# Kernel optimization log

Hardware: AMD Instinct MI355X
Metric: run time of the kernel (lower is better)

## Reference

```python
import jax, jax.numpy as jnp
import numpy as np

H = 8  # hidden size (hardcoded in the module)


def _lstm_scan(x, Wih, Whh, b):
    """Unidirectional LSTM over x:[B,T,I] with PyTorch gate order (i,f,g,o).
    Wih:[4H,I], Whh:[4H,H], b:[4H] (= b_ih + b_hh). Returns h seq [B,T,H]."""
    B = x.shape[0]
    # Precompute input projections for all timesteps in one GEMM: [T,B,4H]
    xg = jnp.einsum('bti,gi->tbg', x, Wih) + b

    def step(carry, xt):
        h, c = carry
        z = xt + h @ Whh.T
        i, f, g, o = jnp.split(z, 4, axis=-1)
        c = jax.nn.sigmoid(f) * c + jax.nn.sigmoid(i) * jnp.tanh(g)
        h = jax.nn.sigmoid(o) * jnp.tanh(c)
        return (h, c), h

    init = (jnp.zeros((B, H), x.dtype), jnp.zeros((B, H), x.dtype))
    _, hs = jax.lax.scan(step, init, xg)  # hs: [T,B,H]
    return jnp.swapaxes(hs, 0, 1)


def _bilstm(x, Wih_f, Whh_f, b_f, Wih_b, Whh_b, b_b):
    fwd = _lstm_scan(x, Wih_f, Whh_f, b_f)
    bwd = _lstm_scan(x[:, ::-1], Wih_b, Whh_b, b_b)[:, ::-1]
    return jnp.concatenate([fwd, bwd], axis=-1)  # [B,T,2H]


def setup_inputs() -> dict:
    key = jax.random.key(0)
    ks = jax.random.split(key, 17)
    s = 1.0 / np.sqrt(H)  # PyTorch uniform(-1/sqrt(H), 1/sqrt(H)) init

    def u(k, shape):
        return jax.random.uniform(k, shape, jnp.float32, -s, s)

    x = jax.random.normal(ks[0], (256, 4096, 8), jnp.float32)
    inp = {'x': x}
    # LSTM params: biases are b_ih + b_hh fused (mathematically identical)
    names = [('Wih1f', (4 * H, 8)), ('Whh1f', (4 * H, H)), ('b1f', (4 * H,)),
             ('Wih1b', (4 * H, 8)), ('Whh1b', (4 * H, H)), ('b1b', (4 * H,)),
             ('Wih2f', (4 * H, 8)), ('Whh2f', (4 * H, H)), ('b2f', (4 * H,)),
             ('Wih2b', (4 * H, 8)), ('Whh2b', (4 * H, H)), ('b2b', (4 * H,)),
             ('W1', (8, 2 * H)), ('bl1', (8,)),
             ('W2', (8, 2 * H)), ('bl2', (8,))]
    for i, (name, shape) in enumerate(names):
        inp[name] = u(ks[i + 1], shape)
    return inp


def reference(x, Wih1f, Whh1f, b1f, Wih1b, Whh1b, b1b,
              Wih2f, Whh2f, b2f, Wih2b, Whh2b, b2b,
              W1, bl1, W2, bl2):
    h1 = _bilstm(x, Wih1f, Whh1f, b1f, Wih1b, Whh1b, b1b)   # [B,T,16]
    y1 = h1 @ W1.T + bl1                                     # [B,T,8]
    h2 = _bilstm(y1, Wih2f, Whh2f, b2f, Wih2b, Whh2b, b2b)  # [B,T,16]
    return h2 @ W2.T + bl2                                   # [B,T,8]
```

## Files before the change

kernel.cpp:

```cpp
#include <hip/hip_runtime.h>

#define T_LEN 4096
#define B_SZ  256

typedef float v2f __attribute__((ext_vector_type(2)));
typedef float v4f __attribute__((ext_vector_type(4)));

__device__ __forceinline__ float fexp2(float x) { return __builtin_amdgcn_exp2f(x); }
__device__ __forceinline__ float frcp(float x)  { return __builtin_amdgcn_rcpf(x); }

template<int S>
__device__ __forceinline__ float rorN(float v) {
    return __int_as_float(__builtin_amdgcn_update_dpp(
        0, __float_as_int(v), 0x120 + S, 0xf, 0xf, true));
}

template<int OFF>
__device__ __forceinline__ v4f aload(const float* p) {
    v4f r;
    asm volatile("global_load_dwordx4 %0, %1, off offset:%2"
                 : "=v"(r) : "v"(p), "i"(OFF) : "memory");
    return r;
}
__device__ __forceinline__ void aatomic(float* p, float v) {
    unsafeAtomicAdd(p, v);
}

__global__ void init_bias_kernel(const float* __restrict__ bl1,
                                 const float* __restrict__ bl2,
                                 float* __restrict__ y1,
                                 float* __restrict__ out)
{
    const long idx = (long)blockIdx.x * blockDim.x + threadIdx.x;
    float4 a1 = make_float4(bl1[0], bl1[1], bl1[2], bl1[3]);
    float4 b1 = make_float4(bl1[4], bl1[5], bl1[6], bl1[7]);
    float4 a2 = make_float4(bl2[0], bl2[1], bl2[2], bl2[3]);
    float4 b2 = make_float4(bl2[4], bl2[5], bl2[6], bl2[7]);
    float4* y4 = (float4*)y1;
    float4* o4 = (float4*)out;
    y4[idx * 2 + 0] = a1;
    y4[idx * 2 + 1] = b1;
    o4[idx * 2 + 0] = a2;
    o4[idx * 2 + 1] = b2;
}

template<int ST>
__device__ __forceinline__ void rec_body(
    const float* x,
    const float* Wih,
    const float* Whh,
    const float* bias,
    const float* Wp,
    int dcol,
    float* y,
    int b0)
{
    const int tid  = threadIdx.x;
    const int cl   = tid & 15;
    const int j    = cl & 7;
    const int half = cl >> 3;
    const int b    = b0 + (tid >> 4);

    const int rA = half * 16 + j;
    const int rB = half * 16 + 8 + j;

    const float NL2E = -1.4426950408889634f;
    const float GSC  = 2.0f * NL2E;
    const float sA   = half ? GSC : NL2E;
    const float sB   = NL2E;
    const float aselA = half ? 2.0f : GSC;
    const float bselA = half ? -1.0f : 0.0f;

    v2f Whk[8], Wik[8];
    float Wcp[8];
    #pragma unroll
    for (int s = 0; s < 8; ++s) {
        const int k = (j - s) & 7;
        Whk[s] = (v2f){Whh[rA * 8 + k] * sA, Whh[rB * 8 + k] * sB};
        Wcp[s] = Wp[j * 16 + dcol + k] * 0.5f;
    }
    #pragma unroll
    for (int k = 0; k < 8; ++k)
        Wik[k] = (v2f){Wih[rA * 8 + k] * sA, Wih[rB * 8 + k] * sB};
    const v2f bpk = (v2f){bias[rA] * sA, bias[rB] * sB};

    const int start = (ST > 0) ? 0 : (T_LEN - 1);
    const float* xp = x + ((long)b * T_LEN + start) * 8;
    float*       wp = y + ((long)b * T_LEN + start) * 8 + j;

    float sc = 0.0f, h = 0.0f;

    auto step = [&](v4f xa, v4f xb, bool doProj) {
        v2f ipA = bpk;
        ipA = __builtin_elementwise_fma(Wik[0], (v2f){xa.x, xa.x}, ipA);
        ipA = __builtin_elementwise_fma(Wik[1], (v2f){xa.y, xa.y}, ipA);
        ipA = __builtin_elementwise_fma(Wik[2], (v2f){xa.z, xa.z}, ipA);
        ipA = __builtin_elementwise_fma(Wik[3], (v2f){xa.w, xa.w}, ipA);
        v2f ipB = Wik[4] * (v2f){xb.x, xb.x};
        ipB = __builtin_elementwise_fma(Wik[5], (v2f){xb.y, xb.y}, ipB);
        ipB = __builtin_elementwise_fma(Wik[6], (v2f){xb.z, xb.z}, ipB);
        ipB = __builtin_elementwise_fma(Wik[7], (v2f){xb.w, xb.w}, ipB);

        float hr0 = h;
        float hr1 = rorN<1>(h);
        float hr2 = rorN<2>(h);
        float hr3 = rorN<3>(h);
        float hr4 = rorN<4>(h);
        float hr5 = rorN<5>(h);
        float hr6 = rorN<6>(h);
        float hr7 = rorN<7>(h);

        v2f cA = __builtin_elementwise_fma(Whk[0], (v2f){hr0, hr0}, ipA);
        cA = __builtin_elementwise_fma(Whk[1], (v2f){hr1, hr1}, cA);
        v2f cB = __builtin_elementwise_fma(Whk[2], (v2f){hr2, hr2}, ipB);
        cB = __builtin_elementwise_fma(Whk[3], (v2f){hr3, hr3}, cB);
        v2f cC = Whk[4] * (v2f){hr4, hr4};
        cC = __builtin_elementwise_fma(Whk[5], (v2f){hr5, hr5}, cC);
        v2f cD = Whk[6] * (v2f){hr6, hr6};
        cD = __builtin_elementwise_fma(Whk[7], (v2f){hr7, hr7}, cD);
        const v2f z = (cA + cB) + (cC + cD);

        if (doProj) {
            float pa = hr0 * Wcp[0];
            pa = fmaf(hr1, Wcp[1], pa);
            pa = fmaf(hr2, Wcp[2], pa);
            pa = fmaf(hr3, Wcp[3], pa);
            pa = fmaf(hr4, Wcp[4], pa);
            pa = fmaf(hr5, Wcp[5], pa);
            pa = fmaf(hr6, Wcp[6], pa);
            pa = fmaf(hr7, Wcp[7], pa);
            aatomic(wp, pa);
            wp += ST * 8;
        }

        const float vA = fmaf(frcp(1.0f + fexp2(z.x)), aselA, bselA);
        const float vB = frcp(1.0f + fexp2(z.y));

        const float pAx = rorN<8>(vA);
        const float pBx = rorN<8>(vB);
        const float gf = half ? pBx : vB;
        const float go = half ? vB  : pBx;

        sc = fmaf(gf, sc, vA * pAx);
        const float th = fmaf(frcp(1.0f + fexp2(sc)), 2.0f, -1.0f);
        h = go * th;
    };

    v4f A0, A1, A2, A3, A4, A5, A6, A7;
    v4f B0, B1, B2, B3, B4, B5, B6, B7;
    v4f C0, C1, C2, C3, C4, C5, C6, C7;

#define AREGS A0, A1, A2, A3, A4, A5, A6, A7
#define BREGS B0, B1, B2, B3, B4, B5, B6, B7
#define CREGS C0, C1, C2, C3, C4, C5, C6, C7

#define LOADM_I(P0, P1, P2, P3, P4, P5, P6, P7)                                \
    P0 = aload<0>(xp);            P1 = aload<16>(xp);                          \
    P2 = aload<ST * 32>(xp);      P3 = aload<ST * 32 + 16>(xp);                \
    P4 = aload<ST * 64>(xp);      P5 = aload<ST * 64 + 16>(xp);                \
    P6 = aload<ST * 96>(xp);      P7 = aload<ST * 96 + 16>(xp);                \
    xp += ST * 32;
#define LOADM(REGS) LOADM_I(REGS)

#define WAITM_I(N, P0, P1, P2, P3, P4, P5, P6, P7)                             \
    asm volatile("s_waitcnt vmcnt(" #N ")"                                     \
        : "+v"(P0), "+v"(P1), "+v"(P2), "+v"(P3),                              \
          "+v"(P4), "+v"(P5), "+v"(P6), "+v"(P7) :: "memory")
#define WAITM(N, REGS) WAITM_I(N, REGS)

#define MACRO4_I(P0, P1, P2, P3, P4, P5, P6, P7, FIRSTPROJ)                    \
    step(P0, P1, FIRSTPROJ);                                                   \
    step(P2, P3, true);                                                        \
    step(P4, P5, true);                                                        \
    step(P6, P7, true);
#define MACRO4(REGS, FIRSTPROJ) MACRO4_I(REGS, FIRSTPROJ)

    asm volatile("s_waitcnt vmcnt(0)" ::: "memory");

    LOADM(AREGS)
    LOADM(BREGS)
    LOADM(CREGS)
    WAITM(16, AREGS); MACRO4(AREGS, false)
    LOADM(AREGS)
    WAITM(19, BREGS); MACRO4(BREGS, true)
    LOADM(BREGS)
    WAITM(23, CREGS); MACRO4(CREGS, true)

    for (int i = 0; i < 339; ++i) {
        LOADM(CREGS) WAITM(24, AREGS); MACRO4(AREGS, true)
        LOADM(AREGS) WAITM(24, BREGS); MACRO4(BREGS, true)
        LOADM(BREGS) WAITM(24, CREGS); MACRO4(CREGS, true)
    }
    LOADM(CREGS)
    WAITM(24, AREGS); MACRO4(AREGS, true)
    LOADM(AREGS)
    WAITM(24, BREGS); MACRO4(BREGS, true)
    WAITM(16, CREGS); MACRO4(CREGS, true)
    WAITM(8,  AREGS); MACRO4(AREGS, true)

#undef LOADM
#undef LOADM_I
#undef MACRO4
#undef MACRO4_I
#undef WAITM
#undef WAITM_I
#undef AREGS
#undef BREGS
#undef CREGS

    {
        float pa = h * Wcp[0];
        pa = fmaf(rorN<1>(h), Wcp[1], pa);
        pa = fmaf(rorN<2>(h), Wcp[2], pa);
        pa = fmaf(rorN<3>(h), Wcp[3], pa);
        pa = fmaf(rorN<4>(h), Wcp[4], pa);
        pa = fmaf(rorN<5>(h), Wcp[5], pa);
        pa = fmaf(rorN<6>(h), Wcp[6], pa);
        pa = fmaf(rorN<7>(h), Wcp[7], pa);
        aatomic(wp, pa);
    }
}

__global__ __launch_bounds__(64, 1)
void lstm_rec_kernel(const float* __restrict__ x,
                     const float* __restrict__ WihF, const float* __restrict__ WhhF,
                     const float* __restrict__ bF,
                     const float* __restrict__ WihB, const float* __restrict__ WhhB,
                     const float* __restrict__ bB,
                     const float* __restrict__ Wp,
                     float* __restrict__ y)
{
    if (blockIdx.x < 64)
        rec_body<1 >(x, WihF, WhhF, bF, Wp, 0, y, 4 * (int)blockIdx.x);
    else
        rec_body<-1>(x, WihB, WhhB, bB, Wp, 8, y, 4 * ((int)blockIdx.x - 64));
}

extern "C" void kernel_launch(void* const* d_in, const int* in_sizes, int n_in,
                              void* d_out, int out_size, void* d_ws, size_t ws_size,
                              hipStream_t stream)
{
    const float* x     = (const float*)d_in[0];
    const float* Wih1f = (const float*)d_in[1];
    const float* Whh1f = (const float*)d_in[2];
    const float* b1f   = (const float*)d_in[3];
    const float* Wih1b = (const float*)d_in[4];
    const float* Whh1b = (const float*)d_in[5];
    const float* b1b   = (const float*)d_in[6];
    const float* Wih2f = (const float*)d_in[7];
    const float* Whh2f = (const float*)d_in[8];
    const float* b2f   = (const float*)d_in[9];
    const float* Wih2b = (const float*)d_in[10];
    const float* Whh2b = (const float*)d_in[11];
    const float* b2b   = (const float*)d_in[12];
    const float* W1    = (const float*)d_in[13];
    const float* bl1   = (const float*)d_in[14];
    const float* W2    = (const float*)d_in[15];
    const float* bl2   = (const float*)d_in[16];

    float* out = (float*)d_out;
    float* y1  = (float*)d_ws;

    const int BT = B_SZ * T_LEN;

    init_bias_kernel<<<BT / 256, 256, 0, stream>>>(bl1, bl2, y1, out);

    lstm_rec_kernel<<<128, 64, 0, stream>>>(x, Wih1f, Whh1f, b1f,
                                            Wih1b, Whh1b, b1b, W1, y1);

    lstm_rec_kernel<<<128, 64, 0, stream>>>(y1, Wih2f, Whh2f, b2f,
                                            Wih2b, Whh2b, b2b, W2, out);
}
```

Baseline: 1.099 ms.

## Split output projection out of recurrent LSTM into separate elementwise kernel

When enough workspace is available, the recurrent kernels stop doing the per-step 8-term projection and atomic adds. Instead they store raw hidden states with plain stores, forward to workspace and backward to the output buffer. A separate fully parallel kernel then applies the linear layer plus bias. This removes atomics and projection math from the latency-bound serial loop, but adds two extra launches and more memory traffic for the intermediate hidden states.

```diff
diff --git a/kernel.cpp b/kernel.cpp
--- a/kernel.cpp
+++ b/kernel.cpp
@@ -24,6 +24,9 @@
 }
 __device__ __forceinline__ void aatomic(float* p, float v) {
     unsafeAtomicAdd(p, v);
+}
+__device__ __forceinline__ void astore(float* p, float v) {
+    asm volatile("global_store_dword %0, %1, off" :: "v"(p), "v"(v) : "memory");
 }
 
 __global__ void init_bias_kernel(const float* __restrict__ bl1,
@@ -44,7 +47,45 @@
     o4[idx * 2 + 1] = b2;
 }
 
-template<int ST>
+__global__ void proj_kernel(const float* __restrict__ Hf,
+                            const float* Hb,
+                            const float* __restrict__ W,
+                            const float* __restrict__ bl,
+                            float* yo)
+{
+    const long idx = (long)blockIdx.x * blockDim.x + threadIdx.x;
+    const float4* f4 = (const float4*)(Hf + idx * 8);
+    const float4* b4 = (const float4*)(Hb + idx * 8);
+    float4 fa = f4[0], fb = f4[1];
+    float4 ba = b4[0], bb = b4[1];
+    float o[8];
+    #pragma unroll
+    for (int d = 0; d < 8; ++d) {
+        float s = bl[d];
+        s = fmaf(fa.x, W[d * 16 + 0], s);
+        s = fmaf(fa.y, W[d * 16 + 1], s);
+        s = fmaf(fa.z, W[d * 16 + 2], s);
+        s = fmaf(fa.w, W[d * 16 + 3], s);
+        s = fmaf(fb.x, W[d * 16 + 4], s);
+        s = fmaf(fb.y, W[d * 16 + 5], s);
+        s = fmaf(fb.z, W[d * 16 + 6], s);
+        s = fmaf(fb.w, W[d * 16 + 7], s);
+        s = fmaf(ba.x, W[d * 16 + 8], s);
+        s = fmaf(ba.y, W[d * 16 + 9], s);
+        s = fmaf(ba.z, W[d * 16 + 10], s);
+        s = fmaf(ba.w, W[d * 16 + 11], s);
+        s = fmaf(bb.x, W[d * 16 + 12], s);
+        s = fmaf(bb.y, W[d * 16 + 13], s);
+        s = fmaf(bb.z, W[d * 16 + 14], s);
+        s = fmaf(bb.w, W[d * 16 + 15], s);
+        o[d] = s;
+    }
+    float4* y4 = (float4*)(yo + idx * 8);
+    y4[0] = make_float4(o[0], o[1], o[2], o[3]);
+    y4[1] = make_float4(o[4], o[5], o[6], o[7]);
+}
+
+template<int ST, bool PROJ>
 __device__ __forceinline__ void rec_body(
     const float* x,
     const float* Wih,
@@ -53,6 +94,7 @@
     const float* Wp,
     int dcol,
     float* y,
+    float* H,
     int b0)
 {
     const int tid  = threadIdx.x;
@@ -77,7 +119,8 @@
     for (int s = 0; s < 8; ++s) {
         const int k = (j - s) & 7;
         Whk[s] = (v2f){Whh[rA * 8 + k] * sA, Whh[rB * 8 + k] * sB};
-        Wcp[s] = Wp[j * 16 + dcol + k] * 0.5f;
+        if constexpr (PROJ)
+            Wcp[s] = Wp[j * 16 + dcol + k] * 0.5f;
     }
     #pragma unroll
     for (int k = 0; k < 8; ++k)
@@ -86,7 +129,10 @@
 
     const int start = (ST > 0) ? 0 : (T_LEN - 1);
     const float* xp = x + ((long)b * T_LEN + start) * 8;
-    float*       wp = y + ((long)b * T_LEN + start) * 8 + j;
+    float* wp = nullptr;
+    float* hp = nullptr;
+    if constexpr (PROJ)  wp = y + ((long)b * T_LEN + start) * 8 + j;
+    if constexpr (!PROJ) hp = H + ((long)b * T_LEN + start) * 8 + j;
 
     float sc = 0.0f, h = 0.0f;
 
@@ -120,17 +166,19 @@
         cD = __builtin_elementwise_fma(Whk[7], (v2f){hr7, hr7}, cD);
         const v2f z = (cA + cB) + (cC + cD);
 
-        if (doProj) {
-            float pa = hr0 * Wcp[0];
-            pa = fmaf(hr1, Wcp[1], pa);
-            pa = fmaf(hr2, Wcp[2], pa);
-            pa = fmaf(hr3, Wcp[3], pa);
-            pa = fmaf(hr4, Wcp[4], pa);
-            pa = fmaf(hr5, Wcp[5], pa);
-            pa = fmaf(hr6, Wcp[6], pa);
-            pa = fmaf(hr7, Wcp[7], pa);
-            aatomic(wp, pa);
-            wp += ST * 8;
+        if constexpr (PROJ) {
+            if (doProj) {
+                float pa = hr0 * Wcp[0];
+                pa = fmaf(hr1, Wcp[1], pa);
+                pa = fmaf(hr2, Wcp[2], pa);
+                pa = fmaf(hr3, Wcp[3], pa);
+                pa = fmaf(hr4, Wcp[4], pa);
+                pa = fmaf(hr5, Wcp[5], pa);
+                pa = fmaf(hr6, Wcp[6], pa);
+                pa = fmaf(hr7, Wcp[7], pa);
+                aatomic(wp, pa);
+                wp += ST * 8;
+            }
         }
 
         const float vA = fmaf(frcp(1.0f + fexp2(z.x)), aselA, bselA);
@@ -144,6 +192,11 @@
         sc = fmaf(gf, sc, vA * pAx);
         const float th = fmaf(frcp(1.0f + fexp2(sc)), 2.0f, -1.0f);
         h = go * th;
+
+        if constexpr (!PROJ) {
+            astore(hp, h);
+            hp += ST * 8;
+        }
     };
 
     v4f A0, A1, A2, A3, A4, A5, A6, A7;
@@ -180,11 +233,20 @@
     LOADM(AREGS)
     LOADM(BREGS)
     LOADM(CREGS)
-    WAITM(16, AREGS); MACRO4(AREGS, false)
-    LOADM(AREGS)
-    WAITM(19, BREGS); MACRO4(BREGS, true)
-    LOADM(BREGS)
-    WAITM(23, CREGS); MACRO4(CREGS, true)
+
+    if constexpr (PROJ) {
+        WAITM(16, AREGS); MACRO4(AREGS, false)
+        LOADM(AREGS)
+        WAITM(19, BREGS); MACRO4(BREGS, true)
+        LOADM(BREGS)
+        WAITM(23, CREGS); MACRO4(CREGS, true)
+    } else {
+        WAITM(16, AREGS); MACRO4(AREGS, true)
+        LOADM(AREGS)
+        WAITM(20, BREGS); MACRO4(BREGS, true)
+        LOADM(BREGS)
+        WAITM(24, CREGS); MACRO4(CREGS, true)
+    }
 
     for (int i = 0; i < 339; ++i) {
         LOADM(CREGS) WAITM(24, AREGS); MACRO4(AREGS, true)
@@ -208,7 +270,7 @@
 #undef BREGS
 #undef CREGS
 
-    {
+    if constexpr (PROJ) {
         float pa = h * Wcp[0];
         pa = fmaf(rorN<1>(h), Wcp[1], pa);
         pa = fmaf(rorN<2>(h), Wcp[2], pa);
@@ -231,9 +293,24 @@
                      float* __restrict__ y)
 {
     if (blockIdx.x < 64)
-        rec_body<1 >(x, WihF, WhhF, bF, Wp, 0, y, 4 * (int)blockIdx.x);
+        rec_body<1,  true>(x, WihF, WhhF, bF, Wp, 0, y, nullptr, 4 * (int)blockIdx.x);
     else
-        rec_body<-1>(x, WihB, WhhB, bB, Wp, 8, y, 4 * ((int)blockIdx.x - 64));
+        rec_body<-1, true>(x, WihB, WhhB, bB, Wp, 8, y, nullptr, 4 * ((int)blockIdx.x - 64));
+}
+
+__global__ __launch_bounds__(64, 1)
+void lstm_rec_np_kernel(const float* __restrict__ x,
+                        const float* __restrict__ WihF, const float* __restrict__ WhhF,
+                        const float* __restrict__ bF,
+                        const float* __restrict__ WihB, const float* __restrict__ WhhB,
+                        const float* __restrict__ bB,
+                        float* __restrict__ Hf,
+                        float* __restrict__ Hb)
+{
+    if (blockIdx.x < 64)
+        rec_body<1,  false>(x, WihF, WhhF, bF, nullptr, 0, nullptr, Hf, 4 * (int)blockIdx.x);
+    else
+        rec_body<-1, false>(x, WihB, WhhB, bB, nullptr, 0, nullptr, Hb, 4 * ((int)blockIdx.x - 64));
 }
 
 extern "C" void kernel_launch(void* const* d_in, const int* in_sizes, int n_in,
@@ -259,15 +336,27 @@
     const float* bl2   = (const float*)d_in[16];
 
     float* out = (float*)d_out;
-    float* y1  = (float*)d_ws;
-
     const int BT = B_SZ * T_LEN;
-
-    init_bias_kernel<<<BT / 256, 256, 0, stream>>>(bl1, bl2, y1, out);
-
-    lstm_rec_kernel<<<128, 64, 0, stream>>>(x, Wih1f, Whh1f, b1f,
-                                            Wih1b, Whh1b, b1b, W1, y1);
-
-    lstm_rec_kernel<<<128, 64, 0, stream>>>(y1, Wih2f, Whh2f, b2f,
-                                            Wih2b, Whh2b, b2b, W2, out);
-}
+    const size_t MB32 = (size_t)32 * 1024 * 1024;
+
+    if (ws_size >= 2 * MB32) {
+        float* ws0 = (float*)d_ws;
+        float* ws1 = (float*)((char*)d_ws + MB32);
+        float* Hb  = out;
+
+        lstm_rec_np_kernel<<<128, 64, 0, stream>>>(x, Wih1f, Whh1f, b1f,
+                                                   Wih1b, Whh1b, b1b, ws0, Hb);
+        proj_kernel<<<BT / 256, 256, 0, stream>>>(ws0, Hb, W1, bl1, ws1);
+        lstm_rec_np_kernel<<<128, 64, 0, stream>>>(ws1, Wih2f, Whh2f, b2f,
+                                                   Wih2b, Whh2b, b2b, ws0, Hb);
+        proj_kernel<<<BT / 256, 256, 0, stream>>>(ws0, Hb, W2, bl2, out);
+    } else {
+        float* y1 = (float*)d_ws;
+
+        init_bias_kernel<<<BT / 256, 256, 0, stream>>>(bl1, bl2, y1, out);
+        lstm_rec_kernel<<<128, 64, 0, stream>>>(x, Wih1f, Whh1f, b1f,
+                                                Wih1b, Whh1b, b1b, W1, y1);
+        lstm_rec_kernel<<<128, 64, 0, stream>>>(y1, Wih2f, Whh2f, b2f,
+                                                Wih2b, Whh2b, b2b, W2, out);
+    }
+}
```

New measurement: 1.071 ms. -2.5%, faster.
